# Kernel optimization log

Hardware: AMD Instinct MI355X
Metric: run time of the kernel (lower is better)

## Reference

```python
import jax, jax.numpy as jnp
import numpy as np
from jax import lax

B, T, N = 256, 2048, 64  # batch, max_seq_len, num_tags


def setup_inputs() -> dict:
    key = jax.random.key(0)
    k1, k2, k3 = jax.random.split(key, 3)
    x = jax.random.normal(k1, (B, T, N), dtype=jnp.float32)
    seq_len = jax.random.randint(k2, (B,), 1, T + 1).astype(jnp.int32)
    trans = (jax.random.normal(k3, (N, N), dtype=jnp.float32) * 0.1)
    return {"x": x, "seq_len": seq_len, "trans": trans}


def reference(x, seq_len, trans):
    # Viterbi decode (tfa.text.crf_decode): returns (tags [B,T] int32, scores [B] float)
    Bv, Tv, Nv = x.shape
    alpha0 = x[:, 0]                                   # [B,N]
    xs = jnp.swapaxes(x[:, 1:], 0, 1)                  # [T-1,B,N]
    valid = jnp.arange(1, Tv)[:, None] < seq_len[None, :]  # [T-1,B]
    ident = jnp.arange(Nv, dtype=jnp.int32)

    def fwd(alpha, inp):
        x_t, v = inp
        # scores[b, prev, cur] = alpha[b, prev] + trans[prev, cur]
        sc = alpha[:, :, None] + trans[None]           # [B,N,N]
        bp = jnp.argmax(sc, axis=1).astype(jnp.int32)  # [B,N] best prev tag per cur
        new_alpha = jnp.max(sc, axis=1) + x_t          # [B,N]
        # steps beyond seq_len: carry state, identity backpointer
        alpha_n = jnp.where(v[:, None], new_alpha, alpha)
        bp = jnp.where(v[:, None], bp, ident[None, :])
        return alpha_n, bp

    alpha_f, bps = lax.scan(fwd, alpha0, (xs, valid))  # bps: [T-1,B,N]
    scores = jnp.max(alpha_f, axis=-1)                 # [B]
    last = jnp.argmax(alpha_f, axis=-1).astype(jnp.int32)  # [B] tag at last step

    def bwd(tag, bp):
        prev = jnp.take_along_axis(bp, tag[:, None], axis=1)[:, 0]
        return prev, tag  # emit tag at step t+1, carry tag at step t

    first, rest = lax.scan(bwd, last, bps, reverse=True)   # rest: [T-1,B]
    tags = jnp.concatenate([first[:, None], jnp.swapaxes(rest, 0, 1)], axis=1)  # [B,T]
    return tags, scores
```

## Files before the change

### kernel.cpp

```cpp
#include <hip/hip_runtime.h>

#define BB 256
#define TT 2048
#define NN 64

__device__ __forceinline__ int dpp_xor1_i(int v) {
  return __builtin_amdgcn_update_dpp(v, v, 0xB1, 0xF, 0xF, true);
}
__device__ __forceinline__ int dpp_xor2_i(int v) {
  return __builtin_amdgcn_update_dpp(v, v, 0x4E, 0xF, 0xF, true);
}
__device__ __forceinline__ float dpp_xor1_f(float v) {
  return __int_as_float(dpp_xor1_i(__float_as_int(v)));
}
__device__ __forceinline__ float dpp_xor2_f(float v) {
  return __int_as_float(dpp_xor2_i(__float_as_int(v)));
}

#define LINK(mq, bq, val, idx)        \
  {                                   \
    float c_ = (val);                 \
    bool g_ = c_ > (mq);              \
    (mq) = g_ ? c_ : (mq);            \
    (bq) = g_ ? (idx) : (bq);         \
  }

__global__ __launch_bounds__(256, 1)
void crf_viterbi_kernel(const float* __restrict__ x,
                        const int* __restrict__ seq_len,
                        const float* __restrict__ trans,
                        float* __restrict__ out) {
  const int b = blockIdx.x;
  const int tid = threadIdx.x;
  const int lane = tid & 63;
  const int w = tid >> 6;
  const int c = lane >> 2;
  const int q = lane & 3;
  const int jc = (w << 4) + c;
  const int iq = q << 4;

  __shared__ __align__(16) float alpha_s[2][NN];
  __shared__ unsigned char bp_s[(TT - 1) * NN];

  const float* xb = x + (size_t)b * TT * NN;
  const int slen = seq_len[b];

  float tc[16];
#pragma unroll
  for (int k = 0; k < 16; ++k) tc[k] = trans[(iq + k) * NN + jc];

  if (w == 0) alpha_s[0][lane] = xb[lane];
  __syncthreads();

  float xn1 = xb[NN + jc];
  float xn2 = xb[2 * NN + jc];

  for (int t = 1; t < slen; ++t) {
    float xv = xn1;
    xn1 = xn2;
    {
      int tn = (t + 2 < TT) ? (t + 2) : (TT - 1);
      xn2 = xb[(size_t)tn * NN + jc];
    }
    const int pr = (t + 1) & 1;
    const int pw = t & 1;

    float4 a0 = *reinterpret_cast<const float4*>(&alpha_s[pr][iq + 0]);
    float4 a1 = *reinterpret_cast<const float4*>(&alpha_s[pr][iq + 4]);
    float4 a2 = *reinterpret_cast<const float4*>(&alpha_s[pr][iq + 8]);
    float4 a3 = *reinterpret_cast<const float4*>(&alpha_s[pr][iq + 12]);

    float m0 = a0.x + tc[0]; int b0 = iq + 0;
    float m1 = a1.x + tc[4]; int b1 = iq + 4;
    float m2 = a2.x + tc[8]; int b2 = iq + 8;
    float m3 = a3.x + tc[12]; int b3 = iq + 12;
    LINK(m0, b0, a0.y + tc[1], iq + 1)
    LINK(m1, b1, a1.y + tc[5], iq + 5)
    LINK(m2, b2, a2.y + tc[9], iq + 9)
    LINK(m3, b3, a3.y + tc[13], iq + 13)
    LINK(m0, b0, a0.z + tc[2], iq + 2)
    LINK(m1, b1, a1.z + tc[6], iq + 6)
    LINK(m2, b2, a2.z + tc[10], iq + 10)
    LINK(m3, b3, a3.z + tc[14], iq + 14)
    LINK(m0, b0, a0.w + tc[3], iq + 3)
    LINK(m1, b1, a1.w + tc[7], iq + 7)
    LINK(m2, b2, a2.w + tc[11], iq + 11)
    LINK(m3, b3, a3.w + tc[15], iq + 15)
    { bool g = m1 > m0; m0 = g ? m1 : m0; b0 = g ? b1 : b0; }
    { bool g = m3 > m2; m2 = g ? m3 : m2; b2 = g ? b3 : b2; }
    { bool g = m2 > m0; m0 = g ? m2 : m0; b0 = g ? b2 : b0; }

    {
      float pv = dpp_xor1_f(m0);
      int pi = dpp_xor1_i(b0);
      bool take = (pv > m0) || (pv == m0 && pi < b0);
      m0 = take ? pv : m0;
      b0 = take ? pi : b0;
    }
    {
      float pv = dpp_xor2_f(m0);
      int pi = dpp_xor2_i(b0);
      bool take = (pv > m0) || (pv == m0 && pi < b0);
      m0 = take ? pv : m0;
      b0 = take ? pi : b0;
    }

    if (q == 0) {
      alpha_s[pw][jc] = m0 + xv;
      bp_s[(t - 1) * NN + jc] = (unsigned char)b0;
    }

    asm volatile("s_waitcnt lgkmcnt(0)\n\ts_barrier" ::: "memory");
  }

  const int pf = (slen - 1) & 1;
  float best = alpha_s[pf][lane];
  int last = lane;
#pragma unroll
  for (int mask = 1; mask < 64; mask <<= 1) {
    float ov = __shfl_xor(best, mask, 64);
    int oi = __shfl_xor(last, mask, 64);
    bool take = (ov > best) || (ov == best && oi < last);
    best = take ? ov : best;
    last = take ? oi : last;
  }
  const float lastf = (float)last;

  for (int t = slen - 1 + tid; t < TT; t += 256) out[b * TT + t] = lastf;

  if (tid == 0) {
    out[BB * TT + b] = best;

    int tag = last;
    for (int t = slen - 2; t >= 0; --t) {
      tag = bp_s[t * NN + tag];
      out[b * TT + t] = (float)tag;
    }
  }
}

extern "C" void kernel_launch(void* const* d_in, const int* in_sizes, int n_in,
                              void* d_out, int out_size, void* d_ws, size_t ws_size,
                              hipStream_t stream) {
  const float* x = (const float*)d_in[0];
  const int* seq_len = (const int*)d_in[1];
  const float* trans = (const float*)d_in[2];
  float* out = (float*)d_out;

  crf_viterbi_kernel<<<BB, 256, 0, stream>>>(x, seq_len, trans, out);
}
```

Baseline: 802.8 us.

## Rotate alpha via DPP across lanes and parallelize backtrace in chunks

Result: no change. 792.9 us (-1.2%).

```diff
diff --git a/kernel.cpp b/kernel.cpp
--- a/kernel.cpp
+++ b/kernel.cpp
@@ -3,27 +3,16 @@
 #define BB 256
 #define TT 2048
 #define NN 64
+#define CHK 512
 
-__device__ __forceinline__ int dpp_xor1_i(int v) {
-  return __builtin_amdgcn_update_dpp(v, v, 0xB1, 0xF, 0xF, true);
+template <int K>
+__device__ __forceinline__ int dpp_ror_i(int v) {
+  return __builtin_amdgcn_update_dpp(0, v, 0x120 | K, 0xF, 0xF, true);
 }
-__device__ __forceinline__ int dpp_xor2_i(int v) {
-  return __builtin_amdgcn_update_dpp(v, v, 0x4E, 0xF, 0xF, true);
+template <int K>
+__device__ __forceinline__ float dpp_ror_f(float v) {
+  return __int_as_float(dpp_ror_i<K>(__float_as_int(v)));
 }
-__device__ __forceinline__ float dpp_xor1_f(float v) {
-  return __int_as_float(dpp_xor1_i(__float_as_int(v)));
-}
-__device__ __forceinline__ float dpp_xor2_f(float v) {
-  return __int_as_float(dpp_xor2_i(__float_as_int(v)));
-}
-
-#define LINK(mq, bq, val, idx)        \
-  {                                   \
-    float c_ = (val);                 \
-    bool g_ = c_ > (mq);              \
-    (mq) = g_ ? c_ : (mq);            \
-    (bq) = g_ ? (idx) : (bq);         \
-  }
 
 __global__ __launch_bounds__(256, 1)
 void crf_viterbi_kernel(const float* __restrict__ x,
@@ -34,20 +23,30 @@
   const int tid = threadIdx.x;
   const int lane = tid & 63;
   const int w = tid >> 6;
-  const int c = lane >> 2;
-  const int q = lane & 3;
+  const int c = lane & 15;
   const int jc = (w << 4) + c;
-  const int iq = q << 4;
 
   __shared__ __align__(16) float alpha_s[2][NN];
   __shared__ unsigned char bp_s[(TT - 1) * NN];
+  __shared__ int map_s[4][NN];
 
   const float* xb = x + (size_t)b * TT * NN;
   const int slen = seq_len[b];
 
-  float tc[16];
+  int idxv[16];
+  idxv[0] = lane;
+  idxv[1] = dpp_ror_i<1>(lane);   idxv[2] = dpp_ror_i<2>(lane);
+  idxv[3] = dpp_ror_i<3>(lane);   idxv[4] = dpp_ror_i<4>(lane);
+  idxv[5] = dpp_ror_i<5>(lane);   idxv[6] = dpp_ror_i<6>(lane);
+  idxv[7] = dpp_ror_i<7>(lane);   idxv[8] = dpp_ror_i<8>(lane);
+  idxv[9] = dpp_ror_i<9>(lane);   idxv[10] = dpp_ror_i<10>(lane);
+  idxv[11] = dpp_ror_i<11>(lane); idxv[12] = dpp_ror_i<12>(lane);
+  idxv[13] = dpp_ror_i<13>(lane); idxv[14] = dpp_ror_i<14>(lane);
+  idxv[15] = dpp_ror_i<15>(lane);
+
+  float tcv[16];
 #pragma unroll
-  for (int k = 0; k < 16; ++k) tc[k] = trans[(iq + k) * NN + jc];
+  for (int k = 0; k < 16; ++k) tcv[k] = trans[idxv[k] * NN + jc];
 
   if (w == 0) alpha_s[0][lane] = xb[lane];
   __syncthreads();
@@ -65,51 +64,44 @@
     const int pr = (t + 1) & 1;
     const int pw = t & 1;
 
-    float4 a0 = *reinterpret_cast<const float4*>(&alpha_s[pr][iq + 0]);
-    float4 a1 = *reinterpret_cast<const float4*>(&alpha_s[pr][iq + 4]);
-    float4 a2 = *reinterpret_cast<const float4*>(&alpha_s[pr][iq + 8]);
-    float4 a3 = *reinterpret_cast<const float4*>(&alpha_s[pr][iq + 12]);
+    float av = alpha_s[pr][lane];
 
-    float m0 = a0.x + tc[0]; int b0 = iq + 0;
-    float m1 = a1.x + tc[4]; int b1 = iq + 4;
-    float m2 = a2.x + tc[8]; int b2 = iq + 8;
-    float m3 = a3.x + tc[12]; int b3 = iq + 12;
-    LINK(m0, b0, a0.y + tc[1], iq + 1)
-    LINK(m1, b1, a1.y + tc[5], iq + 5)
-    LINK(m2, b2, a2.y + tc[9], iq + 9)
-    LINK(m3, b3, a3.y + tc[13], iq + 13)
-    LINK(m0, b0, a0.z + tc[2], iq + 2)
-    LINK(m1, b1, a1.z + tc[6], iq + 6)
-    LINK(m2, b2, a2.z + tc[10], iq + 10)
-    LINK(m3, b3, a3.z + tc[14], iq + 14)
-    LINK(m0, b0, a0.w + tc[3], iq + 3)
-    LINK(m1, b1, a1.w + tc[7], iq + 7)
-    LINK(m2, b2, a2.w + tc[11], iq + 11)
-    LINK(m3, b3, a3.w + tc[15], iq + 15)
+#define CAND(K) (dpp_ror_f<K>(av) + tcv[K])
+#define LNK(K, mq, bq)                                       \
+    {                                                        \
+      float c_ = CAND(K);                                    \
+      bool g_ = c_ > (mq);                                   \
+      (mq) = g_ ? c_ : (mq);                                 \
+      (bq) = g_ ? idxv[K] : (bq);                            \
+    }
+    float m0 = av + tcv[0]; int b0 = idxv[0];
+    float m1 = CAND(4);     int b1 = idxv[4];
+    float m2 = CAND(8);     int b2 = idxv[8];
+    float m3 = CAND(12);    int b3 = idxv[12];
+    LNK(1, m0, b0) LNK(5, m1, b1) LNK(9,  m2, b2) LNK(13, m3, b3)
+    LNK(2, m0, b0) LNK(6, m1, b1) LNK(10, m2, b2) LNK(14, m3, b3)
+    LNK(3, m0, b0) LNK(7, m1, b1) LNK(11, m2, b2) LNK(15, m3, b3)
     { bool g = m1 > m0; m0 = g ? m1 : m0; b0 = g ? b1 : b0; }
     { bool g = m3 > m2; m2 = g ? m3 : m2; b2 = g ? b3 : b2; }
     { bool g = m2 > m0; m0 = g ? m2 : m0; b0 = g ? b2 : b0; }
+#undef LNK
+#undef CAND
 
     {
-      float pv = dpp_xor1_f(m0);
-      int pi = dpp_xor1_i(b0);
-      bool take = (pv > m0) || (pv == m0 && pi < b0);
-      m0 = take ? pv : m0;
-      b0 = take ? pi : b0;
+      float pm = __shfl_xor(m0, 16, 64);
+      int pb = __shfl_xor(b0, 16, 64);
+      bool g = pm > m0; m0 = g ? pm : m0; b0 = g ? pb : b0;
     }
     {
-      float pv = dpp_xor2_f(m0);
-      int pi = dpp_xor2_i(b0);
-      bool take = (pv > m0) || (pv == m0 && pi < b0);
-      m0 = take ? pv : m0;
-      b0 = take ? pi : b0;
+      float pm = __shfl_xor(m0, 32, 64);
+      int pb = __shfl_xor(b0, 32, 64);
+      bool g = pm > m0; m0 = g ? pm : m0; b0 = g ? pb : b0;
     }
 
-    if (q == 0) {
+    if (lane < 16) {
       alpha_s[pw][jc] = m0 + xv;
       bp_s[(t - 1) * NN + jc] = (unsigned char)b0;
     }
-
     asm volatile("s_waitcnt lgkmcnt(0)\n\ts_barrier" ::: "memory");
   }
 
@@ -125,16 +117,32 @@
     last = take ? oi : last;
   }
   const float lastf = (float)last;
+  const int bTT = b * TT;
 
-  for (int t = slen - 1 + tid; t < TT; t += 256) out[b * TT + t] = lastf;
+  for (int t = slen - 1 + tid; t < TT; t += 256) out[bTT + t] = lastf;
+  if (tid == 0) out[BB * TT + b] = best;
 
-  if (tid == 0) {
-    out[BB * TT + b] = best;
+  const int lo = CHK * w;
+  const int hi = ((CHK * (w + 1) - 1) < (slen - 2)) ? (CHK * (w + 1) - 1)
+                                                    : (slen - 2);
+  {
+    int s = lane;
+    for (int r = hi; r >= lo; --r) s = bp_s[r * NN + s];
+    map_s[w][lane] = s;
+  }
+  __syncthreads();
 
-    int tag = last;
-    for (int t = slen - 2; t >= 0; --t) {
-      tag = bp_s[t * NN + tag];
-      out[b * TT + t] = (float)tag;
+  const int e3 = last;
+  const int e2 = map_s[3][e3];
+  const int e1 = map_s[2][e2];
+  const int e0 = map_s[1][e1];
+  const int entry = (w == 3) ? e3 : (w == 2) ? e2 : (w == 1) ? e1 : e0;
+
+  if (lane == 0) {
+    int s = entry;
+    for (int r = hi; r >= lo; --r) {
+      s = bp_s[r * NN + s];
+      out[bTT + r] = (float)s;
     }
   }
 }
```
